# Optimization experiments

Measured on AMD Instinct MI355X. Metric: run time of the kernel, lower is better.

Reference implementation:

```python
import jax, jax.numpy as jnp
import numpy as np

B = 65536
IN = 512
SEQ = 4
LN_EPS = 1e-5


def _ln(x, g, b, eps=LN_EPS):
    # LayerNorm over last dim with affine params
    m = jnp.mean(x, axis=-1, keepdims=True)
    v = jnp.mean((x - m) ** 2, axis=-1, keepdims=True)
    return (x - m) * jax.lax.rsqrt(v + eps) * g + b


def setup_inputs() -> dict:
    key = jax.random.key(0)
    ks = jax.random.split(key, 24)

    def lin(k, shape, fan_in):
        return jax.random.normal(k, shape, jnp.float32) / np.sqrt(fan_in)

    return {
        "x": jax.random.normal(ks[0], (B, IN), jnp.float32),
        "history": jax.random.normal(ks[1], (B, SEQ * IN), jnp.float32),
        # gate network: (seq*in)->64->32
        "g1_w": lin(ks[2], (64, SEQ * IN), SEQ * IN), "g1_b": lin(ks[3], (64,), SEQ * IN),
        "g2_w": lin(ks[4], (32, 64), 64), "g2_b": lin(ks[5], (32,), 64),
        # base modulated layer in->128
        "base_w": lin(ks[6], (128, IN), IN), "base_b": lin(ks[7], (128,), IN),
        "ln1_g": jnp.ones((128,), jnp.float32), "ln1_b": jnp.zeros((128,), jnp.float32),
        # main network: NoisyLinear(eval) 128->64, LN(64), Linear 64->32
        "n1_w": lin(ks[8], (64, 128), 128), "n1_b": lin(ks[9], (64,), 128),
        "ln2_g": jnp.ones((64,), jnp.float32), "ln2_b": jnp.zeros((64,), jnp.float32),
        "m_w": lin(ks[10], (32, 64), 64), "m_b": lin(ks[11], (32,), 64),
        # value stream 32->16->1
        "v1_w": lin(ks[12], (16, 32), 32), "v1_b": lin(ks[13], (16,), 32),
        "v2_w": lin(ks[14], (1, 16), 16), "v2_b": lin(ks[15], (1,), 16),
        # advantage stream 32->16->4 (NoisyLinear in eval mode = mu only)
        "a1_w": lin(ks[16], (16, 32), 32), "a1_b": lin(ks[17], (16,), 32),
        "a2_w": lin(ks[18], (4, 16), 16), "a2_b": lin(ks[19], (4,), 16),
    }


def reference(x, history, g1_w, g1_b, g2_w, g2_b, base_w, base_b, ln1_g, ln1_b,
              n1_w, n1_b, ln2_g, ln2_b, m_w, m_b,
              v1_w, v1_b, v2_w, v2_b, a1_w, a1_b, a2_w, a2_b):
    # gate network
    h = jax.nn.relu(history @ g1_w.T + g1_b)
    gate_values = jax.nn.sigmoid(h @ g2_w.T + g2_b)            # [B, 32]
    mod = 0.7 + 0.3 * jnp.mean(gate_values, axis=1, keepdims=True)  # [B, 1]

    # per-sample scalar weight modulation: bmm(x, (mod*W)^T) == (x @ W^T) * mod
    x_gated = (x @ base_w.T) * mod + base_b                    # [B, 128]
    x_gated = _ln(jax.nn.relu(x_gated), ln1_g, ln1_b)

    # main network (NoisyLinear in eval mode -> mu weights)
    f = jax.nn.relu(x_gated @ n1_w.T + n1_b)
    f = _ln(f, ln2_g, ln2_b)
    features = jax.nn.relu(f @ m_w.T + m_b)                    # [B, 32]

    value = jax.nn.relu(features @ v1_w.T + v1_b) @ v2_w.T + v2_b    # [B, 1]
    advantage = jax.nn.relu(features @ a1_w.T + a1_b) @ a2_w.T + a2_b  # [B, 4]

    q_values = value + (advantage - jnp.mean(advantage, axis=1, keepdims=True))
    return q_values, gate_values
```

## Files before the change

kernel.cpp:

```cpp
#include <hip/hip_runtime.h>
#include <hip/hip_bf16.h>

typedef float f32x4 __attribute__((ext_vector_type(4)));
typedef __bf16 bf16x8 __attribute__((ext_vector_type(8)));
typedef unsigned int u32;
typedef u32 u32x4 __attribute__((ext_vector_type(4)));

#define PK1  0
#define PK2  131072
#define PK3  133120
#define PK4  264192
#define PK5  280576
#define PK6V 284672
#define PK6A 285696

__device__ __forceinline__ f32x4 mfma16(bf16x8 a, bf16x8 b, f32x4 c) {
    return __builtin_amdgcn_mfma_f32_16x16x32_bf16(a, b, c, 0, 0, 0);
}
__device__ __forceinline__ float redsum16(float v) {
    v += __shfl_xor(v, 1); v += __shfl_xor(v, 2);
    v += __shfl_xor(v, 4); v += __shfl_xor(v, 8);
    return v;
}
__device__ __forceinline__ unsigned short bfb(__bf16 b) {
    return __builtin_bit_cast(unsigned short, b);
}
__device__ __forceinline__ bf16x8 cvt8(f32x4 a, f32x4 b) {
    bf16x8 r;
    r[0]=(__bf16)a[0]; r[1]=(__bf16)a[1]; r[2]=(__bf16)a[2]; r[3]=(__bf16)a[3];
    r[4]=(__bf16)b[0]; r[5]=(__bf16)b[1]; r[6]=(__bf16)b[2]; r[7]=(__bf16)b[3];
    return r;
}
__device__ __forceinline__ void split8(f32x4 a, f32x4 b, bf16x8& h, bf16x8& l) {
    #pragma unroll
    for (int e=0;e<4;++e){ __bf16 hb=(__bf16)a[e]; h[e]=hb; l[e]=(__bf16)(a[e]-(float)hb); }
    #pragma unroll
    for (int e=0;e<4;++e){ __bf16 hb=(__bf16)b[e]; h[4+e]=hb; l[4+e]=(__bf16)(b[e]-(float)hb); }
}
__device__ __forceinline__ void unpack8(u32x4 w0, u32x4 w1, bf16x8& h, bf16x8& l) {
    u32 h0=(w0[0]&0xFFFFu)|(w0[1]<<16), h1=(w0[2]&0xFFFFu)|(w0[3]<<16);
    u32 h2=(w1[0]&0xFFFFu)|(w1[1]<<16), h3=(w1[2]&0xFFFFu)|(w1[3]<<16);
    u32 l0=(w0[0]>>16)|(w0[1]&0xFFFF0000u), l1=(w0[2]>>16)|(w0[3]&0xFFFF0000u);
    u32 l2=(w1[0]>>16)|(w1[1]&0xFFFF0000u), l3=(w1[2]>>16)|(w1[3]&0xFFFF0000u);
    u32x4 hv={h0,h1,h2,h3}, lv={l0,l1,l2,l3};
    h=__builtin_bit_cast(bf16x8,hv); l=__builtin_bit_cast(bf16x8,lv);
}

__device__ __forceinline__ void pack_plain(const float* __restrict__ W, __bf16* __restrict__ dst,
                                           int i, int K, int Nn) {
    int e=i&7, lane=(i>>3)&63, p=i>>9;
    int n=p%Nn, t=p/Nn;
    float v = W[(size_t)(n*16+(lane&15))*K + t*32 + (lane>>4)*8 + e];
    dst[i] = (__bf16)v;
}
__device__ __forceinline__ void pack_hilo(const float* __restrict__ W, __bf16* __restrict__ dst,
                                          int i, int K, int Nn) {
    int e=i&7, lane=(i>>3)&63, p=i>>9;
    int n=p%Nn, t=p/Nn;
    float v = W[(size_t)(n*16+(lane&15))*K + t*32 + (lane>>4)*8 + e];
    __bf16 h = (__bf16)v;
    dst[p*1024 + (i&511)]       = h;
    dst[p*1024 + 512 + (i&511)] = (__bf16)(v - (float)h);
}
__global__ void pack_weights(const float* g1w, const float* g2w, const float* bw,
                             const float* n1w, const float* mw, const float* v1w,
                             const float* a1w, __bf16* wsb) {
    int gi = blockIdx.x*256 + threadIdx.x;
    if      (gi < 131072) pack_plain(g1w, wsb+PK1, gi,          2048, 4);
    else if (gi < 133120) pack_plain(g2w, wsb+PK2, gi-131072,   64,   2);
    else if (gi < 198656) pack_hilo (bw,  wsb+PK3, gi-133120,   512,  8);
    else if (gi < 206848) pack_hilo (n1w, wsb+PK4, gi-198656,   128,  4);
    else if (gi < 208896) pack_hilo (mw,  wsb+PK5, gi-206848,   64,   2);
    else if (gi < 209408) pack_hilo (v1w, wsb+PK6V, gi-208896,  32,   1);
    else if (gi < 209920) pack_hilo (a1w, wsb+PK6A, gi-209408,  32,   1);
}

__global__ __launch_bounds__(256, 4)
void gated_dqn_main(const float* __restrict__ x,   const float* __restrict__ hist,
                    const float* __restrict__ g1b, const float* __restrict__ g2b,
                    const float* __restrict__ bb,  const float* __restrict__ ln1g,
                    const float* __restrict__ ln1b,const float* __restrict__ n1b,
                    const float* __restrict__ ln2g,const float* __restrict__ ln2b,
                    const float* __restrict__ mb,  const float* __restrict__ v1b,
                    const float* __restrict__ v2w, const float* __restrict__ v2b,
                    const float* __restrict__ a1b, const float* __restrict__ a2w,
                    const float* __restrict__ a2b, const __bf16* __restrict__ wsb,
                    float* __restrict__ qout, float* __restrict__ gateout)
{
    __shared__ __align__(16) float scr[4][2112];
    const int tid = threadIdx.x, lane = tid & 63, wv = tid >> 6;
    const int qq = lane >> 4, c = lane & 15;
    const int r0 = (blockIdx.x*4 + wv)*16;
    float*  myA = scr[wv];
    u32*    my  = (u32*)myA;
    __bf16* myb = (__bf16*)myA;
    const int swc = ((c >> 1) & 3) << 3;
    const int srl = lane >> 3, scl = lane & 7;

    f32x4 acc[4] = {};
    {
        const float* aRow0 = hist + (size_t)(r0 + srl)*2048 + scl*4;
        const float* aRow1 = hist + (size_t)(r0 + 8 + srl)*2048 + scl*4;
        f32x4 rg[8];
        #pragma unroll
        for (int q = 0; q < 4; ++q) {
            rg[q]   = *(const f32x4*)(aRow0 + q*32);
            rg[4+q] = *(const f32x4*)(aRow1 + q*32);
        }
        const __bf16* bB = wsb + PK1 + lane*8;
        bf16x8 cb0 = *(const bf16x8*)(bB),      cb1 = *(const bf16x8*)(bB+512);
        bf16x8 cb2 = *(const bf16x8*)(bB+1024), cb3 = *(const bf16x8*)(bB+1536);
        for (int g = 0; g < 16; ++g) {
            #pragma unroll
            for (int q = 0; q < 4; ++q) {
                *(f32x4*)&myA[srl*132     + q*32 + scl*4] = rg[q];
                *(f32x4*)&myA[(8+srl)*132 + q*32 + scl*4] = rg[4+q];
            }
            if (g + 1 < 16) {
                #pragma unroll
                for (int q = 0; q < 4; ++q) {
                    rg[q]   = *(const f32x4*)(aRow0 + (g+1)*128 + q*32);
                    rg[4+q] = *(const f32x4*)(aRow1 + (g+1)*128 + q*32);
                }
            }
            #pragma unroll
            for (int t = 0; t < 4; ++t) {
                int ktn = g*4 + t + 1; if (ktn > 63) ktn = 63;
                const __bf16* btn = bB + (size_t)ktn*2048;
                bf16x8 nb0 = *(const bf16x8*)(btn),      nb1 = *(const bf16x8*)(btn+512);
                bf16x8 nb2 = *(const bf16x8*)(btn+1024), nb3 = *(const bf16x8*)(btn+1536);
                f32x4 lo = *(const f32x4*)&myA[c*132 + t*32 + qq*8];
                f32x4 hi = *(const f32x4*)&myA[c*132 + t*32 + qq*8 + 4];
                bf16x8 af = cvt8(lo, hi);
                acc[0] = mfma16(af, cb0, acc[0]); acc[1] = mfma16(af, cb1, acc[1]);
                acc[2] = mfma16(af, cb2, acc[2]); acc[3] = mfma16(af, cb3, acc[3]);
                cb0 = nb0; cb1 = nb1; cb2 = nb2; cb3 = nb3;
            }
        }
        #pragma unroll
        for (int n = 0; n < 4; ++n) {
            float bv = g1b[n*16 + c];
            #pragma unroll
            for (int j = 0; j < 4; ++j) {
                int r = qq*4 + j, col = n*16 + c;
                myb[r*64 + (col ^ (((r>>1)&3)<<3))] = (__bf16)fmaxf(acc[n][j] + bv, 0.0f);
            }
        }
    }

    float mj[4];
    {
        const __bf16* bB = wsb + PK2 + lane*8;
        bf16x8 a0 = *(const bf16x8*)&myb[c*64 + ((qq*8) ^ swc)];
        bf16x8 a1 = *(const bf16x8*)&myb[c*64 + ((32 + qq*8) ^ swc)];
        bf16x8 b00 = *(const bf16x8*)(bB),      b01 = *(const bf16x8*)(bB+512);
        bf16x8 b10 = *(const bf16x8*)(bB+1024), b11 = *(const bf16x8*)(bB+1536);
        f32x4 ag0 = {}, ag1 = {};
        ag0 = mfma16(a0, b00, ag0); ag1 = mfma16(a0, b01, ag1);
        ag0 = mfma16(a1, b10, ag0); ag1 = mfma16(a1, b11, ag1);
        float s[4] = {0,0,0,0};
        #pragma unroll
        for (int n = 0; n < 2; ++n) {
            float bv = g2b[n*16 + c];
            f32x4 ag = n ? ag1 : ag0;
            #pragma unroll
            for (int j = 0; j < 4; ++j) {
                float gv = 1.0f / (1.0f + __expf(-(ag[j] + bv)));
                gateout[(size_t)(r0 + qq*4 + j)*32 + n*16 + c] = gv;
                s[j] += gv;
            }
        }
        #pragma unroll
        for (int j = 0; j < 4; ++j)
            mj[j] = 0.7f + 0.3f * redsum16(s[j]) * (1.0f/32.0f);
    }

    f32x4 a3[8] = {};
    {
        const float* aRow0 = x + (size_t)(r0 + srl)*512 + scl*4;
        const float* aRow1 = x + (size_t)(r0 + 8 + srl)*512 + scl*4;
        f32x4 rg[8];
        #pragma unroll
        for (int q = 0; q < 4; ++q) {
            rg[q]   = *(const f32x4*)(aRow0 + q*32);
            rg[4+q] = *(const f32x4*)(aRow1 + q*32);
        }
        for (int g = 0; g < 4; ++g) {
            #pragma unroll
            for (int q = 0; q < 4; ++q) {
                *(f32x4*)&myA[srl*132     + q*32 + scl*4] = rg[q];
                *(f32x4*)&myA[(8+srl)*132 + q*32 + scl*4] = rg[4+q];
            }
            if (g + 1 < 4) {
                #pragma unroll
                for (int q = 0; q < 4; ++q) {
                    rg[q]   = *(const f32x4*)(aRow0 + (g+1)*128 + q*32);
                    rg[4+q] = *(const f32x4*)(aRow1 + (g+1)*128 + q*32);
                }
            }
            #pragma unroll
            for (int t = 0; t < 4; ++t) {
                f32x4 lo = *(const f32x4*)&myA[c*132 + t*32 + qq*8];
                f32x4 hi = *(const f32x4*)&myA[c*132 + t*32 + qq*8 + 4];
                bf16x8 ah, al; split8(lo, hi, ah, al);
                int kt = g*4 + t;
                #pragma unroll
                for (int half = 0; half < 2; ++half) {
                    const __bf16* bt = wsb + PK3 + (size_t)(kt*16 + half*8)*512 + lane*8;
                    #pragma unroll
                    for (int n = 0; n < 4; ++n) {
                        bf16x8 bh = *(const bf16x8*)(bt + n*1024);
                        f32x4 a = a3[half*4 + n];
                        a = mfma16(ah, bh, a); a = mfma16(al, bh, a);
                        a3[half*4 + n] = a;
                    }
                }
            }
        }
        float s[4] = {0,0,0,0}, ss[4] = {0,0,0,0};
        #pragma unroll
        for (int n = 0; n < 8; ++n) {
            float bv = bb[n*16 + c];
            #pragma unroll
            for (int j = 0; j < 4; ++j) {
                float v = fmaxf(a3[n][j]*mj[j] + bv, 0.0f);
                a3[n][j] = v; s[j] += v; ss[j] += v*v;
            }
        }
        float mean[4], rstd[4];
        #pragma unroll
        for (int j = 0; j < 4; ++j) {
            float t = redsum16(s[j]), t2 = redsum16(ss[j]);
            float m = t * (1.0f/128.0f);
            mean[j] = m; rstd[j] = rsqrtf(t2*(1.0f/128.0f) - m*m + 1e-5f);
        }
        #pragma unroll
        for (int n = 0; n < 8; ++n) {
            float g = ln1g[n*16 + c], b2 = ln1b[n*16 + c];
            #pragma unroll
            for (int j = 0; j < 4; ++j) {
                int r = qq*4 + j, col = n*16 + c;
                float y = (a3[n][j] - mean[j]) * rstd[j] * g + b2;
                __bf16 hb = (__bf16)y; __bf16 lb = (__bf16)(y - (float)hb);
                my[r*128 + (col ^ (((r>>1)&3)<<3))] = (u32)bfb(hb) | ((u32)bfb(lb) << 16);
            }
        }
    }

    f32x4 a4[4] = {};
    {
        const __bf16* bB = wsb + PK4 + lane*8;
        #pragma unroll
        for (int t = 0; t < 4; ++t) {
            int base = c*128 + ((t*32 + qq*8) ^ swc);
            u32x4 w0 = *(const u32x4*)&my[base], w1 = *(const u32x4*)&my[base + 4];
            bf16x8 ah, al; unpack8(w0, w1, ah, al);
            const __bf16* bt = bB + t*4096;
            #pragma unroll
            for (int n = 0; n < 4; ++n) {
                bf16x8 bh = *(const bf16x8*)(bt + n*1024);
                f32x4 a = a4[n];
                a = mfma16(ah, bh, a); a = mfma16(al, bh, a);
                a4[n] = a;
            }
        }
        float s[4] = {0,0,0,0}, ss[4] = {0,0,0,0};
        #pragma unroll
        for (int n = 0; n < 4; ++n) {
            float bv = n1b[n*16 + c];
            #pragma unroll
            for (int j = 0; j < 4; ++j) {
                float v = fmaxf(a4[n][j] + bv, 0.0f);
                a4[n][j] = v; s[j] += v; ss[j] += v*v;
            }
        }
        float mean[4], rstd[4];
        #pragma unroll
        for (int j = 0; j < 4; ++j) {
            float t = redsum16(s[j]), t2 = redsum16(ss[j]);
            float m = t * (1.0f/64.0f);
            mean[j] = m; rstd[j] = rsqrtf(t2*(1.0f/64.0f) - m*m + 1e-5f);
        }
        #pragma unroll
        for (int n = 0; n < 4; ++n) {
            float g = ln2g[n*16 + c], b2 = ln2b[n*16 + c];
            #pragma unroll
            for (int j = 0; j < 4; ++j) {
                int r = qq*4 + j, col = n*16 + c;
                float y = (a4[n][j] - mean[j]) * rstd[j] * g + b2;
                __bf16 hb = (__bf16)y; __bf16 lb = (__bf16)(y - (float)hb);
                my[r*64 + (col ^ (((r>>1)&3)<<3))] = (u32)bfb(hb) | ((u32)bfb(lb) << 16);
            }
        }
    }

    {
        const __bf16* bB = wsb + PK5 + lane*8;
        f32x4 a5[2] = {};
        #pragma unroll
        for (int t = 0; t < 2; ++t) {
            int base = c*64 + ((t*32 + qq*8) ^ swc);
            u32x4 w0 = *(const u32x4*)&my[base], w1 = *(const u32x4*)&my[base + 4];
            bf16x8 ah, al; unpack8(w0, w1, ah, al);
            const __bf16* bt = bB + t*2048;
            #pragma unroll
            for (int n = 0; n < 2; ++n) {
                bf16x8 bh = *(const bf16x8*)(bt + n*1024);
                f32x4 a = a5[n];
                a = mfma16(ah, bh, a); a = mfma16(al, bh, a);
                a5[n] = a;
            }
        }
        #pragma unroll
        for (int n = 0; n < 2; ++n) {
            float bv = mb[n*16 + c];
            #pragma unroll
            for (int j = 0; j < 4; ++j) {
                int r = qq*4 + j, col = n*16 + c;
                float v = fmaxf(a5[n][j] + bv, 0.0f);
                __bf16 hb = (__bf16)v; __bf16 lb = (__bf16)(v - (float)hb);
                my[r*32 + (col ^ (((r>>1)&3)<<3))] = (u32)bfb(hb) | ((u32)bfb(lb) << 16);
            }
        }
    }

    {
        int base = c*32 + ((qq*8) ^ swc);
        u32x4 w0 = *(const u32x4*)&my[base], w1 = *(const u32x4*)&my[base + 4];
        bf16x8 ah, al; unpack8(w0, w1, ah, al);
        const __bf16* bv_ = wsb + PK6V + lane*8;
        const __bf16* ba_ = wsb + PK6A + lane*8;
        bf16x8 vh  = *(const bf16x8*)(bv_);
        bf16x8 ahw = *(const bf16x8*)(ba_);
        f32x4 av = {}, aa = {};
        av = mfma16(ah, vh, av);  av = mfma16(al, vh, av);
        aa = mfma16(ah, ahw, aa); aa = mfma16(al, ahw, aa);
        float v1bc = v1b[c], a1bc = a1b[c], w2 = v2w[c];
        float vb2 = v2b[0];
        float aw0 = a2w[c], aw1 = a2w[16+c], aw2 = a2w[32+c], aw3 = a2w[48+c];
        float ab0 = a2b[0], ab1 = a2b[1], ab2 = a2b[2], ab3 = a2b[3];
        #pragma unroll
        for (int j = 0; j < 4; ++j) {
            float hv = fmaxf(av[j] + v1bc, 0.0f);
            float ha = fmaxf(aa[j] + a1bc, 0.0f);
            float val = redsum16(hv * w2) + vb2;
            float d0 = redsum16(ha * aw0) + ab0;
            float d1 = redsum16(ha * aw1) + ab1;
            float d2 = redsum16(ha * aw2) + ab2;
            float d3 = redsum16(ha * aw3) + ab3;
            float ma = 0.25f * (d0 + d1 + d2 + d3);
            if (c == 0) {
                f32x4 qv = {val + d0 - ma, val + d1 - ma, val + d2 - ma, val + d3 - ma};
                *(f32x4*)(qout + (size_t)(r0 + qq*4 + j)*4) = qv;
            }
        }
    }
}

extern "C" void kernel_launch(void* const* d_in, const int* in_sizes, int n_in,
                              void* d_out, int out_size, void* d_ws, size_t ws_size,
                              hipStream_t stream) {
    (void)in_sizes; (void)n_in; (void)ws_size; (void)out_size;
    const float* x    = (const float*)d_in[0];
    const float* hist = (const float*)d_in[1];
    const float* g1w  = (const float*)d_in[2];
    const float* g1b  = (const float*)d_in[3];
    const float* g2w  = (const float*)d_in[4];
    const float* g2b  = (const float*)d_in[5];
    const float* bw   = (const float*)d_in[6];
    const float* bb   = (const float*)d_in[7];
    const float* ln1g = (const float*)d_in[8];
    const float* ln1b = (const float*)d_in[9];
    const float* n1w  = (const float*)d_in[10];
    const float* n1b  = (const float*)d_in[11];
    const float* ln2g = (const float*)d_in[12];
    const float* ln2b = (const float*)d_in[13];
    const float* mw   = (const float*)d_in[14];
    const float* mb   = (const float*)d_in[15];
    const float* v1w  = (const float*)d_in[16];
    const float* v1b  = (const float*)d_in[17];
    const float* v2w  = (const float*)d_in[18];
    const float* v2b  = (const float*)d_in[19];
    const float* a1w  = (const float*)d_in[20];
    const float* a1b  = (const float*)d_in[21];
    const float* a2w  = (const float*)d_in[22];
    const float* a2b  = (const float*)d_in[23];
    __bf16* wsb = (__bf16*)d_ws;
    float* qout = (float*)d_out;
    float* gateout = qout + (size_t)65536 * 4;

    pack_weights<<<dim3(820), dim3(256), 0, stream>>>(g1w, g2w, bw, n1w, mw, v1w, a1w, wsb);
    gated_dqn_main<<<dim3(1024), dim3(256), 0, stream>>>(
        x, hist, g1b, g2b, bb, ln1g, ln1b, n1b, ln2g, ln2b, mb,
        v1b, v2w, v2b, a1b, a2w, a2b, wsb, qout, gateout);
}
```

Measured before the change: 172.9 us.

## Process 32 rows per wave to reuse weight fragments across two row tiles

Each wave now computes two 16-row tiles, so every B-fragment (weight) load feeds two MFMA chains across all layers. The activation staging switches to 16 row-loads per lane and drops the XOR swizzle in favor of padded LDS rows. The grid is halved and launch bounds reduced to 2, with larger per-wave LDS and register footprints, trading occupancy for less weight traffic and more instruction-level parallelism.

```diff
diff --git a/kernel.cpp b/kernel.cpp
--- a/kernel.cpp
+++ b/kernel.cpp
@@ -75,7 +75,7 @@
     else if (gi < 209920) pack_hilo (a1w, wsb+PK6A, gi-209408,  32,   1);
 }
 
-__global__ __launch_bounds__(256, 4)
+__global__ __launch_bounds__(256, 2)
 void gated_dqn_main(const float* __restrict__ x,   const float* __restrict__ hist,
                     const float* __restrict__ g1b, const float* __restrict__ g2b,
                     const float* __restrict__ bb,  const float* __restrict__ ln1g,
@@ -87,41 +87,32 @@
                     const float* __restrict__ a2b, const __bf16* __restrict__ wsb,
                     float* __restrict__ qout, float* __restrict__ gateout)
 {
-    __shared__ __align__(16) float scr[4][2112];
+    __shared__ __align__(16) u32 scr[4][4224];
     const int tid = threadIdx.x, lane = tid & 63, wv = tid >> 6;
     const int qq = lane >> 4, c = lane & 15;
-    const int r0 = (blockIdx.x*4 + wv)*16;
-    float*  myA = scr[wv];
-    u32*    my  = (u32*)myA;
-    __bf16* myb = (__bf16*)myA;
-    const int swc = ((c >> 1) & 3) << 3;
-    const int srl = lane >> 3, scl = lane & 7;
-
-    f32x4 acc[4] = {};
-    {
-        const float* aRow0 = hist + (size_t)(r0 + srl)*2048 + scl*4;
-        const float* aRow1 = hist + (size_t)(r0 + 8 + srl)*2048 + scl*4;
-        f32x4 rg[8];
-        #pragma unroll
-        for (int q = 0; q < 4; ++q) {
-            rg[q]   = *(const f32x4*)(aRow0 + q*32);
-            rg[4+q] = *(const f32x4*)(aRow1 + q*32);
-        }
+    const int r0 = (blockIdx.x*4 + wv)*32;
+    u32*    my  = scr[wv];
+    float*  myA = (float*)my;
+    __bf16* myb = (__bf16*)my;
+    const int sr2 = lane >> 5, sc2 = lane & 31;
+
+    f32x4 acc1[2][4] = {};
+    {
+        const float* aBase = hist + (size_t)(r0 + sr2*16)*2048 + sc2*4;
+        f32x4 rg[16];
+        #pragma unroll
+        for (int i = 0; i < 16; ++i) rg[i] = *(const f32x4*)(aBase + (size_t)i*2048);
         const __bf16* bB = wsb + PK1 + lane*8;
         bf16x8 cb0 = *(const bf16x8*)(bB),      cb1 = *(const bf16x8*)(bB+512);
         bf16x8 cb2 = *(const bf16x8*)(bB+1024), cb3 = *(const bf16x8*)(bB+1536);
         for (int g = 0; g < 16; ++g) {
             #pragma unroll
-            for (int q = 0; q < 4; ++q) {
-                *(f32x4*)&myA[srl*132     + q*32 + scl*4] = rg[q];
-                *(f32x4*)&myA[(8+srl)*132 + q*32 + scl*4] = rg[4+q];
-            }
+            for (int i = 0; i < 16; ++i)
+                *(f32x4*)&myA[(i + sr2*16)*132 + sc2*4] = rg[i];
             if (g + 1 < 16) {
                 #pragma unroll
-                for (int q = 0; q < 4; ++q) {
-                    rg[q]   = *(const f32x4*)(aRow0 + (g+1)*128 + q*32);
-                    rg[4+q] = *(const f32x4*)(aRow1 + (g+1)*128 + q*32);
-                }
+                for (int i = 0; i < 16; ++i)
+                    rg[i] = *(const f32x4*)(aBase + (size_t)i*2048 + (g+1)*128);
             }
             #pragma unroll
             for (int t = 0; t < 4; ++t) {
@@ -129,229 +120,263 @@
                 const __bf16* btn = bB + (size_t)ktn*2048;
                 bf16x8 nb0 = *(const bf16x8*)(btn),      nb1 = *(const bf16x8*)(btn+512);
                 bf16x8 nb2 = *(const bf16x8*)(btn+1024), nb3 = *(const bf16x8*)(btn+1536);
-                f32x4 lo = *(const f32x4*)&myA[c*132 + t*32 + qq*8];
-                f32x4 hi = *(const f32x4*)&myA[c*132 + t*32 + qq*8 + 4];
-                bf16x8 af = cvt8(lo, hi);
-                acc[0] = mfma16(af, cb0, acc[0]); acc[1] = mfma16(af, cb1, acc[1]);
-                acc[2] = mfma16(af, cb2, acc[2]); acc[3] = mfma16(af, cb3, acc[3]);
+                #pragma unroll
+                for (int rt = 0; rt < 2; ++rt) {
+                    f32x4 lo = *(const f32x4*)&myA[(rt*16 + c)*132 + t*32 + qq*8];
+                    f32x4 hi = *(const f32x4*)&myA[(rt*16 + c)*132 + t*32 + qq*8 + 4];
+                    bf16x8 af = cvt8(lo, hi);
+                    acc1[rt][0] = mfma16(af, cb0, acc1[rt][0]);
+                    acc1[rt][1] = mfma16(af, cb1, acc1[rt][1]);
+                    acc1[rt][2] = mfma16(af, cb2, acc1[rt][2]);
+                    acc1[rt][3] = mfma16(af, cb3, acc1[rt][3]);
+                }
                 cb0 = nb0; cb1 = nb1; cb2 = nb2; cb3 = nb3;
             }
         }
         #pragma unroll
-        for (int n = 0; n < 4; ++n) {
-            float bv = g1b[n*16 + c];
-            #pragma unroll
-            for (int j = 0; j < 4; ++j) {
-                int r = qq*4 + j, col = n*16 + c;
-                myb[r*64 + (col ^ (((r>>1)&3)<<3))] = (__bf16)fmaxf(acc[n][j] + bv, 0.0f);
-            }
-        }
-    }
-
-    float mj[4];
+        for (int rt = 0; rt < 2; ++rt)
+            #pragma unroll
+            for (int n = 0; n < 4; ++n) {
+                float bv = g1b[n*16 + c];
+                #pragma unroll
+                for (int j = 0; j < 4; ++j) {
+                    int r = rt*16 + qq*4 + j;
+                    myb[r*136 + n*16 + c] = (__bf16)fmaxf(acc1[rt][n][j] + bv, 0.0f);
+                }
+            }
+    }
+
+    float mj[2][4];
     {
         const __bf16* bB = wsb + PK2 + lane*8;
-        bf16x8 a0 = *(const bf16x8*)&myb[c*64 + ((qq*8) ^ swc)];
-        bf16x8 a1 = *(const bf16x8*)&myb[c*64 + ((32 + qq*8) ^ swc)];
         bf16x8 b00 = *(const bf16x8*)(bB),      b01 = *(const bf16x8*)(bB+512);
         bf16x8 b10 = *(const bf16x8*)(bB+1024), b11 = *(const bf16x8*)(bB+1536);
-        f32x4 ag0 = {}, ag1 = {};
-        ag0 = mfma16(a0, b00, ag0); ag1 = mfma16(a0, b01, ag1);
-        ag0 = mfma16(a1, b10, ag0); ag1 = mfma16(a1, b11, ag1);
-        float s[4] = {0,0,0,0};
-        #pragma unroll
-        for (int n = 0; n < 2; ++n) {
-            float bv = g2b[n*16 + c];
-            f32x4 ag = n ? ag1 : ag0;
-            #pragma unroll
-            for (int j = 0; j < 4; ++j) {
-                float gv = 1.0f / (1.0f + __expf(-(ag[j] + bv)));
-                gateout[(size_t)(r0 + qq*4 + j)*32 + n*16 + c] = gv;
-                s[j] += gv;
-            }
-        }
-        #pragma unroll
-        for (int j = 0; j < 4; ++j)
-            mj[j] = 0.7f + 0.3f * redsum16(s[j]) * (1.0f/32.0f);
-    }
-
-    f32x4 a3[8] = {};
-    {
-        const float* aRow0 = x + (size_t)(r0 + srl)*512 + scl*4;
-        const float* aRow1 = x + (size_t)(r0 + 8 + srl)*512 + scl*4;
-        f32x4 rg[8];
-        #pragma unroll
-        for (int q = 0; q < 4; ++q) {
-            rg[q]   = *(const f32x4*)(aRow0 + q*32);
-            rg[4+q] = *(const f32x4*)(aRow1 + q*32);
-        }
+        #pragma unroll
+        for (int rt = 0; rt < 2; ++rt) {
+            bf16x8 a0 = *(const bf16x8*)&myb[(rt*16 + c)*136 + qq*8];
+            bf16x8 a1 = *(const bf16x8*)&myb[(rt*16 + c)*136 + 32 + qq*8];
+            f32x4 ag0 = {}, ag1 = {};
+            ag0 = mfma16(a0, b00, ag0); ag1 = mfma16(a0, b01, ag1);
+            ag0 = mfma16(a1, b10, ag0); ag1 = mfma16(a1, b11, ag1);
+            float s[4] = {0,0,0,0};
+            #pragma unroll
+            for (int n = 0; n < 2; ++n) {
+                float bv = g2b[n*16 + c];
+                f32x4 ag = n ? ag1 : ag0;
+                #pragma unroll
+                for (int j = 0; j < 4; ++j) {
+                    float gv = 1.0f / (1.0f + __expf(-(ag[j] + bv)));
+                    gateout[(size_t)(r0 + rt*16 + qq*4 + j)*32 + n*16 + c] = gv;
+                    s[j] += gv;
+                }
+            }
+            #pragma unroll
+            for (int j = 0; j < 4; ++j)
+                mj[rt][j] = 0.7f + 0.3f * redsum16(s[j]) * (1.0f/32.0f);
+        }
+    }
+
+    f32x4 a3[2][8] = {};
+    {
+        const float* aBase = x + (size_t)(r0 + sr2*16)*512 + sc2*4;
+        f32x4 rg[16];
+        #pragma unroll
+        for (int i = 0; i < 16; ++i) rg[i] = *(const f32x4*)(aBase + (size_t)i*512);
         for (int g = 0; g < 4; ++g) {
             #pragma unroll
-            for (int q = 0; q < 4; ++q) {
-                *(f32x4*)&myA[srl*132     + q*32 + scl*4] = rg[q];
-                *(f32x4*)&myA[(8+srl)*132 + q*32 + scl*4] = rg[4+q];
-            }
+            for (int i = 0; i < 16; ++i)
+                *(f32x4*)&myA[(i + sr2*16)*132 + sc2*4] = rg[i];
             if (g + 1 < 4) {
                 #pragma unroll
-                for (int q = 0; q < 4; ++q) {
-                    rg[q]   = *(const f32x4*)(aRow0 + (g+1)*128 + q*32);
-                    rg[4+q] = *(const f32x4*)(aRow1 + (g+1)*128 + q*32);
-                }
+                for (int i = 0; i < 16; ++i)
+                    rg[i] = *(const f32x4*)(aBase + (size_t)i*512 + (g+1)*128);
             }
             #pragma unroll
             for (int t = 0; t < 4; ++t) {
-                f32x4 lo = *(const f32x4*)&myA[c*132 + t*32 + qq*8];
-                f32x4 hi = *(const f32x4*)&myA[c*132 + t*32 + qq*8 + 4];
-                bf16x8 ah, al; split8(lo, hi, ah, al);
                 int kt = g*4 + t;
+                bf16x8 ah[2], al[2];
+                #pragma unroll
+                for (int rt = 0; rt < 2; ++rt) {
+                    f32x4 lo = *(const f32x4*)&myA[(rt*16 + c)*132 + t*32 + qq*8];
+                    f32x4 hi = *(const f32x4*)&myA[(rt*16 + c)*132 + t*32 + qq*8 + 4];
+                    split8(lo, hi, ah[rt], al[rt]);
+                }
                 #pragma unroll
                 for (int half = 0; half < 2; ++half) {
                     const __bf16* bt = wsb + PK3 + (size_t)(kt*16 + half*8)*512 + lane*8;
                     #pragma unroll
                     for (int n = 0; n < 4; ++n) {
                         bf16x8 bh = *(const bf16x8*)(bt + n*1024);
-                        f32x4 a = a3[half*4 + n];
-                        a = mfma16(ah, bh, a); a = mfma16(al, bh, a);
-                        a3[half*4 + n] = a;
+                        #pragma unroll
+                        for (int rt = 0; rt < 2; ++rt) {
+                            f32x4 a = a3[rt][half*4 + n];
+                            a = mfma16(ah[rt], bh, a); a = mfma16(al[rt], bh, a);
+                            a3[rt][half*4 + n] = a;
+                        }
                     }
                 }
             }
         }
-        float s[4] = {0,0,0,0}, ss[4] = {0,0,0,0};
-        #pragma unroll
-        for (int n = 0; n < 8; ++n) {
-            float bv = bb[n*16 + c];
+        #pragma unroll
+        for (int rt = 0; rt < 2; ++rt) {
+            float s[4] = {0,0,0,0}, ss[4] = {0,0,0,0};
+            #pragma unroll
+            for (int n = 0; n < 8; ++n) {
+                float bv = bb[n*16 + c];
+                #pragma unroll
+                for (int j = 0; j < 4; ++j) {
+                    float v = fmaxf(a3[rt][n][j]*mj[rt][j] + bv, 0.0f);
+                    a3[rt][n][j] = v; s[j] += v; ss[j] += v*v;
+                }
+            }
+            float mean[4], rstd[4];
             #pragma unroll
             for (int j = 0; j < 4; ++j) {
-                float v = fmaxf(a3[n][j]*mj[j] + bv, 0.0f);
-                a3[n][j] = v; s[j] += v; ss[j] += v*v;
-            }
-        }
-        float mean[4], rstd[4];
-        #pragma unroll
-        for (int j = 0; j < 4; ++j) {
-            float t = redsum16(s[j]), t2 = redsum16(ss[j]);
-            float m = t * (1.0f/128.0f);
-            mean[j] = m; rstd[j] = rsqrtf(t2*(1.0f/128.0f) - m*m + 1e-5f);
-        }
-        #pragma unroll
-        for (int n = 0; n < 8; ++n) {
-            float g = ln1g[n*16 + c], b2 = ln1b[n*16 + c];
-            #pragma unroll
-            for (int j = 0; j < 4; ++j) {
-                int r = qq*4 + j, col = n*16 + c;
-                float y = (a3[n][j] - mean[j]) * rstd[j] * g + b2;
-                __bf16 hb = (__bf16)y; __bf16 lb = (__bf16)(y - (float)hb);
-                my[r*128 + (col ^ (((r>>1)&3)<<3))] = (u32)bfb(hb) | ((u32)bfb(lb) << 16);
-            }
-        }
-    }
-
-    f32x4 a4[4] = {};
+                float t = redsum16(s[j]), t2 = redsum16(ss[j]);
+                float m = t * (1.0f/128.0f);
+                mean[j] = m; rstd[j] = rsqrtf(t2*(1.0f/128.0f) - m*m + 1e-5f);
+            }
+            #pragma unroll
+            for (int n = 0; n < 8; ++n) {
+                float g = ln1g[n*16 + c], b2 = ln1b[n*16 + c];
+                #pragma unroll
+                for (int j = 0; j < 4; ++j) {
+                    int r = rt*16 + qq*4 + j;
+                    float y = (a3[rt][n][j] - mean[j]) * rstd[j] * g + b2;
+                    __bf16 hb = (__bf16)y; __bf16 lb = (__bf16)(y - (float)hb);
+                    my[r*132 + n*16 + c] = (u32)bfb(hb) | ((u32)bfb(lb) << 16);
+                }
+            }
+        }
+    }
+
+    f32x4 a4[2][4] = {};
     {
         const __bf16* bB = wsb + PK4 + lane*8;
         #pragma unroll
         for (int t = 0; t < 4; ++t) {
-            int base = c*128 + ((t*32 + qq*8) ^ swc);
-            u32x4 w0 = *(const u32x4*)&my[base], w1 = *(const u32x4*)&my[base + 4];
-            bf16x8 ah, al; unpack8(w0, w1, ah, al);
+            bf16x8 ah[2], al[2];
+            #pragma unroll
+            for (int rt = 0; rt < 2; ++rt) {
+                int base = (rt*16 + c)*132 + t*32 + qq*8;
+                u32x4 w0 = *(const u32x4*)&my[base], w1 = *(const u32x4*)&my[base + 4];
+                unpack8(w0, w1, ah[rt], al[rt]);
+            }
             const __bf16* bt = bB + t*4096;
             #pragma unroll
             for (int n = 0; n < 4; ++n) {
                 bf16x8 bh = *(const bf16x8*)(bt + n*1024);
-                f32x4 a = a4[n];
-                a = mfma16(ah, bh, a); a = mfma16(al, bh, a);
-                a4[n] = a;
-            }
-        }
-        float s[4] = {0,0,0,0}, ss[4] = {0,0,0,0};
-        #pragma unroll
-        for (int n = 0; n < 4; ++n) {
-            float bv = n1b[n*16 + c];
+                #pragma unroll
+                for (int rt = 0; rt < 2; ++rt) {
+                    f32x4 a = a4[rt][n];
+                    a = mfma16(ah[rt], bh, a); a = mfma16(al[rt], bh, a);
+                    a4[rt][n] = a;
+                }
+            }
+        }
+        #pragma unroll
+        for (int rt = 0; rt < 2; ++rt) {
+            float s[4] = {0,0,0,0}, ss[4] = {0,0,0,0};
+            #pragma unroll
+            for (int n = 0; n < 4; ++n) {
+                float bv = n1b[n*16 + c];
+                #pragma unroll
+                for (int j = 0; j < 4; ++j) {
+                    float v = fmaxf(a4[rt][n][j] + bv, 0.0f);
+                    a4[rt][n][j] = v; s[j] += v; ss[j] += v*v;
+                }
+            }
+            float mean[4], rstd[4];
             #pragma unroll
             for (int j = 0; j < 4; ++j) {
-                float v = fmaxf(a4[n][j] + bv, 0.0f);
-                a4[n][j] = v; s[j] += v; ss[j] += v*v;
-            }
-        }
-        float mean[4], rstd[4];
-        #pragma unroll
-        for (int j = 0; j < 4; ++j) {
-            float t = redsum16(s[j]), t2 = redsum16(ss[j]);
-            float m = t * (1.0f/64.0f);
-            mean[j] = m; rstd[j] = rsqrtf(t2*(1.0f/64.0f) - m*m + 1e-5f);
-        }
-        #pragma unroll
-        for (int n = 0; n < 4; ++n) {
-            float g = ln2g[n*16 + c], b2 = ln2b[n*16 + c];
-            #pragma unroll
-            for (int j = 0; j < 4; ++j) {
-                int r = qq*4 + j, col = n*16 + c;
-                float y = (a4[n][j] - mean[j]) * rstd[j] * g + b2;
-                __bf16 hb = (__bf16)y; __bf16 lb = (__bf16)(y - (float)hb);
-                my[r*64 + (col ^ (((r>>1)&3)<<3))] = (u32)bfb(hb) | ((u32)bfb(lb) << 16);
+                float t = redsum16(s[j]), t2 = redsum16(ss[j]);
+                float m = t * (1.0f/64.0f);
+                mean[j] = m; rstd[j] = rsqrtf(t2*(1.0f/64.0f) - m*m + 1e-5f);
+            }
+            #pragma unroll
+            for (int n = 0; n < 4; ++n) {
+                float g = ln2g[n*16 + c], b2 = ln2b[n*16 + c];
+                #pragma unroll
+                for (int j = 0; j < 4; ++j) {
+                    int r = rt*16 + qq*4 + j;
+                    float y = (a4[rt][n][j] - mean[j]) * rstd[j] * g + b2;
+                    __bf16 hb = (__bf16)y; __bf16 lb = (__bf16)(y - (float)hb);
+                    my[r*132 + n*16 + c] = (u32)bfb(hb) | ((u32)bfb(lb) << 16);
+                }
             }
         }
     }
 
     {
         const __bf16* bB = wsb + PK5 + lane*8;
-        f32x4 a5[2] = {};
+        f32x4 a5[2][2] = {};
         #pragma unroll
         for (int t = 0; t < 2; ++t) {
-            int base = c*64 + ((t*32 + qq*8) ^ swc);
-            u32x4 w0 = *(const u32x4*)&my[base], w1 = *(const u32x4*)&my[base + 4];
-            bf16x8 ah, al; unpack8(w0, w1, ah, al);
+            bf16x8 ah[2], al[2];
+            #pragma unroll
+            for (int rt = 0; rt < 2; ++rt) {
+                int base = (rt*16 + c)*132 + t*32 + qq*8;
+                u32x4 w0 = *(const u32x4*)&my[base], w1 = *(const u32x4*)&my[base + 4];
+                unpack8(w0, w1, ah[rt], al[rt]);
+            }
             const __bf16* bt = bB + t*2048;
             #pragma unroll
             for (int n = 0; n < 2; ++n) {
                 bf16x8 bh = *(const bf16x8*)(bt + n*1024);
-                f32x4 a = a5[n];
-                a = mfma16(ah, bh, a); a = mfma16(al, bh, a);
-                a5[n] = a;
-            }
-        }
-        #pragma unroll
-        for (int n = 0; n < 2; ++n) {
-            float bv = mb[n*16 + c];
-            #pragma unroll
-            for (int j = 0; j < 4; ++j) {
-                int r = qq*4 + j, col = n*16 + c;
-                float v = fmaxf(a5[n][j] + bv, 0.0f);
-                __bf16 hb = (__bf16)v; __bf16 lb = (__bf16)(v - (float)hb);
-                my[r*32 + (col ^ (((r>>1)&3)<<3))] = (u32)bfb(hb) | ((u32)bfb(lb) << 16);
-            }
-        }
-    }
-
-    {
-        int base = c*32 + ((qq*8) ^ swc);
-        u32x4 w0 = *(const u32x4*)&my[base], w1 = *(const u32x4*)&my[base + 4];
-        bf16x8 ah, al; unpack8(w0, w1, ah, al);
+                #pragma unroll
+                for (int rt = 0; rt < 2; ++rt) {
+                    f32x4 a = a5[rt][n];
+                    a = mfma16(ah[rt], bh, a); a = mfma16(al[rt], bh, a);
+                    a5[rt][n] = a;
+                }
+            }
+        }
+        #pragma unroll
+        for (int rt = 0; rt < 2; ++rt)
+            #pragma unroll
+            for (int n = 0; n < 2; ++n) {
+                float bv = mb[n*16 + c];
+                #pragma unroll
+                for (int j = 0; j < 4; ++j) {
+                    int r = rt*16 + qq*4 + j;
+                    float v = fmaxf(a5[rt][n][j] + bv, 0.0f);
+                    __bf16 hb = (__bf16)v; __bf16 lb = (__bf16)(v - (float)hb);
+                    my[r*132 + n*16 + c] = (u32)bfb(hb) | ((u32)bfb(lb) << 16);
+                }
+            }
+    }
+
+    {
         const __bf16* bv_ = wsb + PK6V + lane*8;
         const __bf16* ba_ = wsb + PK6A + lane*8;
         bf16x8 vh  = *(const bf16x8*)(bv_);
         bf16x8 ahw = *(const bf16x8*)(ba_);
-        f32x4 av = {}, aa = {};
-        av = mfma16(ah, vh, av);  av = mfma16(al, vh, av);
-        aa = mfma16(ah, ahw, aa); aa = mfma16(al, ahw, aa);
         float v1bc = v1b[c], a1bc = a1b[c], w2 = v2w[c];
         float vb2 = v2b[0];
         float aw0 = a2w[c], aw1 = a2w[16+c], aw2 = a2w[32+c], aw3 = a2w[48+c];
         float ab0 = a2b[0], ab1 = a2b[1], ab2 = a2b[2], ab3 = a2b[3];
         #pragma unroll
-        for (int j = 0; j < 4; ++j) {
-            float hv = fmaxf(av[j] + v1bc, 0.0f);
-            float ha = fmaxf(aa[j] + a1bc, 0.0f);
-            float val = redsum16(hv * w2) + vb2;
-            float d0 = redsum16(ha * aw0) + ab0;
-            float d1 = redsum16(ha * aw1) + ab1;
-            float d2 = redsum16(ha * aw2) + ab2;
-            float d3 = redsum16(ha * aw3) + ab3;
-            float ma = 0.25f * (d0 + d1 + d2 + d3);
-            if (c == 0) {
-                f32x4 qv = {val + d0 - ma, val + d1 - ma, val + d2 - ma, val + d3 - ma};
-                *(f32x4*)(qout + (size_t)(r0 + qq*4 + j)*4) = qv;
+        for (int rt = 0; rt < 2; ++rt) {
+            int base = (rt*16 + c)*132 + qq*8;
+            u32x4 w0 = *(const u32x4*)&my[base], w1 = *(const u32x4*)&my[base + 4];
+            bf16x8 ah, al; unpack8(w0, w1, ah, al);
+            f32x4 av = {}, aa = {};
+            av = mfma16(ah, vh, av);  av = mfma16(al, vh, av);
+            aa = mfma16(ah, ahw, aa); aa = mfma16(al, ahw, aa);
+            #pragma unroll
+            for (int j = 0; j < 4; ++j) {
+                float hv = fmaxf(av[j] + v1bc, 0.0f);
+                float ha = fmaxf(aa[j] + a1bc, 0.0f);
+                float val = redsum16(hv * w2) + vb2;
+                float d0 = redsum16(ha * aw0) + ab0;
+                float d1 = redsum16(ha * aw1) + ab1;
+                float d2 = redsum16(ha * aw2) + ab2;
+                float d3 = redsum16(ha * aw3) + ab3;
+                float ma = 0.25f * (d0 + d1 + d2 + d3);
+                if (c == 0) {
+                    f32x4 qv = {val + d0 - ma, val + d1 - ma, val + d2 - ma, val + d3 - ma};
+                    *(f32x4*)(qout + (size_t)(r0 + rt*16 + qq*4 + j)*4) = qv;
+                }
             }
         }
     }
@@ -390,7 +415,7 @@
     float* gateout = qout + (size_t)65536 * 4;
 
     pack_weights<<<dim3(820), dim3(256), 0, stream>>>(g1w, g2w, bw, n1w, mw, v1w, a1w, wsb);
-    gated_dqn_main<<<dim3(1024), dim3(256), 0, stream>>>(
+    gated_dqn_main<<<dim3(512), dim3(256), 0, stream>>>(
         x, hist, g1b, g2b, bb, ln1g, ln1b, n1b, ln2g, ln2b, mb,
         v1b, v2w, v2b, a1b, a2w, a2b, wsb, qout, gateout);
 }
```

After: 175.5 us. About the same (+1.5%).

## Stream history and x tiles into LDS with async global_load_lds double-buffering

Applied to the files above, without the earlier changes.

Replaces the register-staged global→LDS copies of the history and x row tiles with direct global_load_lds transfers into a double-buffered, XOR-swizzled LDS layout. Explicit vmcnt waits overlap the next chunk's load with the current chunk's MFMAs, and the loops are fully unrolled with B fragments loaded per step. The aim is to cut VGPR pressure and the store/load round trip through registers, making the kernel more memory-streaming friendly. It depends on hand-placed waitcnt counts staying correct alongside the compiler's own B-fragment loads. It also drops the previous one-step-ahead B prefetch.

```diff
diff --git a/kernel.cpp b/kernel.cpp
--- a/kernel.cpp
+++ b/kernel.cpp
@@ -44,6 +44,11 @@
     u32 l2=(w1[0]>>16)|(w1[1]&0xFFFF0000u), l3=(w1[2]>>16)|(w1[3]&0xFFFF0000u);
     u32x4 hv={h0,h1,h2,h3}, lv={l0,l1,l2,l3};
     h=__builtin_bit_cast(bf16x8,hv); l=__builtin_bit_cast(bf16x8,lv);
+}
+__device__ __forceinline__ void gl16(const void* g, void* l) {
+    __builtin_amdgcn_global_load_lds(
+        (const __attribute__((address_space(1))) void*)g,
+        (__attribute__((address_space(3))) void*)l, 16, 0, 0);
 }
 
 __device__ __forceinline__ void pack_plain(const float* __restrict__ W, __bf16* __restrict__ dst,
@@ -90,69 +95,72 @@
     __shared__ __align__(16) float scr[4][2112];
     const int tid = threadIdx.x, lane = tid & 63, wv = tid >> 6;
     const int qq = lane >> 4, c = lane & 15;
+    const int c7 = c & 7;
     const int r0 = (blockIdx.x*4 + wv)*16;
     float*  myA = scr[wv];
     u32*    my  = (u32*)myA;
-    __bf16* myb = (__bf16*)myA;
+    char*   ldsA = (char*)myA;
     const int swc = ((c >> 1) & 3) << 3;
-    const int srl = lane >> 3, scl = lane & 7;
 
     f32x4 acc[4] = {};
     {
-        const float* aRow0 = hist + (size_t)(r0 + srl)*2048 + scl*4;
-        const float* aRow1 = hist + (size_t)(r0 + 8 + srl)*2048 + scl*4;
-        f32x4 rg[8];
-        #pragma unroll
-        for (int q = 0; q < 4; ++q) {
-            rg[q]   = *(const f32x4*)(aRow0 + q*32);
-            rg[4+q] = *(const f32x4*)(aRow1 + q*32);
-        }
+        const int glr = lane >> 4, gls = lane & 15;
+        const float* gA[4];
+        #pragma unroll
+        for (int i = 0; i < 4; ++i) {
+            int lr = i*4 + glr;
+            gA[i] = hist + (size_t)(r0 + lr)*2048 + (gls ^ (lr & 7))*4;
+        }
+        #pragma unroll
+        for (int i = 0; i < 4; ++i) gl16(gA[i], ldsA + i*1024);
         const __bf16* bB = wsb + PK1 + lane*8;
-        bf16x8 cb0 = *(const bf16x8*)(bB),      cb1 = *(const bf16x8*)(bB+512);
-        bf16x8 cb2 = *(const bf16x8*)(bB+1024), cb3 = *(const bf16x8*)(bB+1536);
-        for (int g = 0; g < 16; ++g) {
-            #pragma unroll
-            for (int q = 0; q < 4; ++q) {
-                *(f32x4*)&myA[srl*132     + q*32 + scl*4] = rg[q];
-                *(f32x4*)&myA[(8+srl)*132 + q*32 + scl*4] = rg[4+q];
-            }
-            if (g + 1 < 16) {
+        #pragma unroll
+        for (int t = 0; t < 32; ++t) {
+            bf16x8 Bf[2][4];
+            #pragma unroll
+            for (int ktl = 0; ktl < 2; ++ktl)
                 #pragma unroll
-                for (int q = 0; q < 4; ++q) {
-                    rg[q]   = *(const f32x4*)(aRow0 + (g+1)*128 + q*32);
-                    rg[4+q] = *(const f32x4*)(aRow1 + (g+1)*128 + q*32);
-                }
-            }
-            #pragma unroll
-            for (int t = 0; t < 4; ++t) {
-                int ktn = g*4 + t + 1; if (ktn > 63) ktn = 63;
-                const __bf16* btn = bB + (size_t)ktn*2048;
-                bf16x8 nb0 = *(const bf16x8*)(btn),      nb1 = *(const bf16x8*)(btn+512);
-                bf16x8 nb2 = *(const bf16x8*)(btn+1024), nb3 = *(const bf16x8*)(btn+1536);
-                f32x4 lo = *(const f32x4*)&myA[c*132 + t*32 + qq*8];
-                f32x4 hi = *(const f32x4*)&myA[c*132 + t*32 + qq*8 + 4];
+                for (int n = 0; n < 4; ++n)
+                    Bf[ktl][n] = *(const bf16x8*)(bB + (size_t)(t*2 + ktl)*2048 + n*512);
+            if (t + 1 < 32) {
+                char* dst = ldsA + ((t+1)&1)*4096;
+                #pragma unroll
+                for (int i = 0; i < 4; ++i) gl16(gA[i] + (t+1)*64, dst + i*1024);
+                asm volatile("s_waitcnt vmcnt(4)" ::: "memory");
+            } else {
+                asm volatile("s_waitcnt vmcnt(0)" ::: "memory");
+            }
+            const float* buf = myA + (t&1)*1024;
+            #pragma unroll
+            for (int ktl = 0; ktl < 2; ++ktl) {
+                int k0 = ktl*8 + qq*2;
+                f32x4 lo = *(const f32x4*)&buf[c*64 + ((k0    ) ^ c7)*4];
+                f32x4 hi = *(const f32x4*)&buf[c*64 + ((k0 + 1) ^ c7)*4];
                 bf16x8 af = cvt8(lo, hi);
-                acc[0] = mfma16(af, cb0, acc[0]); acc[1] = mfma16(af, cb1, acc[1]);
-                acc[2] = mfma16(af, cb2, acc[2]); acc[3] = mfma16(af, cb3, acc[3]);
-                cb0 = nb0; cb1 = nb1; cb2 = nb2; cb3 = nb3;
-            }
-        }
+                acc[0] = mfma16(af, Bf[ktl][0], acc[0]);
+                acc[1] = mfma16(af, Bf[ktl][1], acc[1]);
+                acc[2] = mfma16(af, Bf[ktl][2], acc[2]);
+                acc[3] = mfma16(af, Bf[ktl][3], acc[3]);
+            }
+        }
+        __bf16* hB = (__bf16*)(myA + 1024);
         #pragma unroll
         for (int n = 0; n < 4; ++n) {
             float bv = g1b[n*16 + c];
             #pragma unroll
             for (int j = 0; j < 4; ++j) {
                 int r = qq*4 + j, col = n*16 + c;
-                myb[r*64 + (col ^ (((r>>1)&3)<<3))] = (__bf16)fmaxf(acc[n][j] + bv, 0.0f);
+                hB[r*64 + (col ^ (((r>>1)&3)<<3))] = (__bf16)fmaxf(acc[n][j] + bv, 0.0f);
             }
         }
     }
 
     float mj[4];
     {
+        const __bf16* hB = (const __bf16*)(myA + 1024);
         const __bf16* bB = wsb + PK2 + lane*8;
-        bf16x8 a0 = *(const bf16x8*)&myb[c*64 + ((qq*8) ^ swc)];
-        bf16x8 a1 = *(const bf16x8*)&myb[c*64 + ((32 + qq*8) ^ swc)];
+        bf16x8 a0 = *(const bf16x8*)&hB[c*64 + ((qq*8) ^ swc)];
+        bf16x8 a1 = *(const bf16x8*)&hB[c*64 + ((32 + qq*8) ^ swc)];
         bf16x8 b00 = *(const bf16x8*)(bB),      b01 = *(const bf16x8*)(bB+512);
         bf16x8 b10 = *(const bf16x8*)(bB+1024), b11 = *(const bf16x8*)(bB+1536);
         f32x4 ag0 = {}, ag1 = {};
@@ -177,44 +185,37 @@
 
     f32x4 a3[8] = {};
     {
-        const float* aRow0 = x + (size_t)(r0 + srl)*512 + scl*4;
-        const float* aRow1 = x + (size_t)(r0 + 8 + srl)*512 + scl*4;
-        f32x4 rg[8];
-        #pragma unroll
-        for (int q = 0; q < 4; ++q) {
-            rg[q]   = *(const f32x4*)(aRow0 + q*32);
-            rg[4+q] = *(const f32x4*)(aRow1 + q*32);
-        }
-        for (int g = 0; g < 4; ++g) {
-            #pragma unroll
-            for (int q = 0; q < 4; ++q) {
-                *(f32x4*)&myA[srl*132     + q*32 + scl*4] = rg[q];
-                *(f32x4*)&myA[(8+srl)*132 + q*32 + scl*4] = rg[4+q];
-            }
-            if (g + 1 < 4) {
+        const int glr3 = lane >> 3, gls3 = lane & 7;
+        const float* gX[2];
+        #pragma unroll
+        for (int i = 0; i < 2; ++i) {
+            int lr = i*8 + glr3;
+            gX[i] = x + (size_t)(r0 + lr)*512 + (gls3 ^ (lr & 7))*4;
+        }
+        #pragma unroll
+        for (int i = 0; i < 2; ++i) gl16(gX[i], ldsA + i*1024);
+        #pragma unroll
+        for (int t = 0; t < 16; ++t) {
+            bf16x8 Bh[8];
+            #pragma unroll
+            for (int n = 0; n < 8; ++n)
+                Bh[n] = *(const bf16x8*)(wsb + PK3 + (size_t)(t*16 + n*2)*512 + lane*8);
+            if (t + 1 < 16) {
+                char* dst = ldsA + ((t+1)&1)*2048;
                 #pragma unroll
-                for (int q = 0; q < 4; ++q) {
-                    rg[q]   = *(const f32x4*)(aRow0 + (g+1)*128 + q*32);
-                    rg[4+q] = *(const f32x4*)(aRow1 + (g+1)*128 + q*32);
-                }
-            }
-            #pragma unroll
-            for (int t = 0; t < 4; ++t) {
-                f32x4 lo = *(const f32x4*)&myA[c*132 + t*32 + qq*8];
-                f32x4 hi = *(const f32x4*)&myA[c*132 + t*32 + qq*8 + 4];
-                bf16x8 ah, al; split8(lo, hi, ah, al);
-                int kt = g*4 + t;
-                #pragma unroll
-                for (int half = 0; half < 2; ++half) {
-                    const __bf16* bt = wsb + PK3 + (size_t)(kt*16 + half*8)*512 + lane*8;
-                    #pragma unroll
-                    for (int n = 0; n < 4; ++n) {
-                        bf16x8 bh = *(const bf16x8*)(bt + n*1024);
-                        f32x4 a = a3[half*4 + n];
-                        a = mfma16(ah, bh, a); a = mfma16(al, bh, a);
-                        a3[half*4 + n] = a;
-                    }
-                }
+                for (int i = 0; i < 2; ++i) gl16(gX[i] + (t+1)*32, dst + i*1024);
+                asm volatile("s_waitcnt vmcnt(2)" ::: "memory");
+            } else {
+                asm volatile("s_waitcnt vmcnt(0)" ::: "memory");
+            }
+            const float* buf = myA + (t&1)*512;
+            f32x4 lo = *(const f32x4*)&buf[c*32 + ((qq*2    ) ^ c7)*4];
+            f32x4 hi = *(const f32x4*)&buf[c*32 + ((qq*2 + 1) ^ c7)*4];
+            bf16x8 ah, al; split8(lo, hi, ah, al);
+            #pragma unroll
+            for (int n = 0; n < 8; ++n) {
+                a3[n] = mfma16(ah, Bh[n], a3[n]);
+                a3[n] = mfma16(al, Bh[n], a3[n]);
             }
         }
         float s[4] = {0,0,0,0}, ss[4] = {0,0,0,0};
```

Result: slower. 186.7 us (+8.0%).

## Widen staged chunks, row-per-load global reads, and loop two tiles per block

Applied to the files above, without the earlier changes.

The input staging for history and x now loads 256-float chunks, with one full row segment per instruction across the wavefront (16 rows of 1 KB contiguous each), instead of 128-float chunks split across 8 lanes per row. The LDS stride becomes 260 floats, so the per-wave scratch roughly doubles. Each block now processes two 16-row tiles per wave in a loop, with the grid halved to 512 and launch bounds relaxed to 2 blocks per SM. The aim is more bytes in flight per load and fewer staging iterations for the bandwidth-bound history read. In exchange, the larger LDS footprint and register buffer (16 f32x4) reduce occupancy.

```diff
diff --git a/kernel.cpp b/kernel.cpp
--- a/kernel.cpp
+++ b/kernel.cpp
@@ -13,6 +13,8 @@
 #define PK5  280576
 #define PK6V 284672
 #define PK6A 285696
+
+#define ASTR 260
 
 __device__ __forceinline__ f32x4 mfma16(bf16x8 a, bf16x8 b, f32x4 c) {
     return __builtin_amdgcn_mfma_f32_16x16x32_bf16(a, b, c, 0, 0, 0);
@@ -75,7 +77,7 @@
     else if (gi < 209920) pack_hilo (a1w, wsb+PK6A, gi-209408,  32,   1);
 }
 
-__global__ __launch_bounds__(256, 4)
+__global__ __launch_bounds__(256, 2)
 void gated_dqn_main(const float* __restrict__ x,   const float* __restrict__ hist,
                     const float* __restrict__ g1b, const float* __restrict__ g2b,
                     const float* __restrict__ bb,  const float* __restrict__ ln1g,
@@ -87,50 +89,43 @@
                     const float* __restrict__ a2b, const __bf16* __restrict__ wsb,
                     float* __restrict__ qout, float* __restrict__ gateout)
 {
-    __shared__ __align__(16) float scr[4][2112];
+    __shared__ __align__(16) float scr[4][16*ASTR];
     const int tid = threadIdx.x, lane = tid & 63, wv = tid >> 6;
     const int qq = lane >> 4, c = lane & 15;
-    const int r0 = (blockIdx.x*4 + wv)*16;
     float*  myA = scr[wv];
     u32*    my  = (u32*)myA;
     __bf16* myb = (__bf16*)myA;
     const int swc = ((c >> 1) & 3) << 3;
-    const int srl = lane >> 3, scl = lane & 7;
+
+    for (int it = 0; it < 2; ++it) {
+    const int r0 = ((it*512 + blockIdx.x)*4 + wv)*16;
 
     f32x4 acc[4] = {};
     {
-        const float* aRow0 = hist + (size_t)(r0 + srl)*2048 + scl*4;
-        const float* aRow1 = hist + (size_t)(r0 + 8 + srl)*2048 + scl*4;
-        f32x4 rg[8];
-        #pragma unroll
-        for (int q = 0; q < 4; ++q) {
-            rg[q]   = *(const f32x4*)(aRow0 + q*32);
-            rg[4+q] = *(const f32x4*)(aRow1 + q*32);
-        }
+        const float* aG = hist + (size_t)r0*2048 + lane*4;
+        f32x4 rg[16];
+        #pragma unroll
+        for (int i = 0; i < 16; ++i) rg[i] = *(const f32x4*)(aG + (size_t)i*2048);
         const __bf16* bB = wsb + PK1 + lane*8;
         bf16x8 cb0 = *(const bf16x8*)(bB),      cb1 = *(const bf16x8*)(bB+512);
         bf16x8 cb2 = *(const bf16x8*)(bB+1024), cb3 = *(const bf16x8*)(bB+1536);
-        for (int g = 0; g < 16; ++g) {
-            #pragma unroll
-            for (int q = 0; q < 4; ++q) {
-                *(f32x4*)&myA[srl*132     + q*32 + scl*4] = rg[q];
-                *(f32x4*)&myA[(8+srl)*132 + q*32 + scl*4] = rg[4+q];
-            }
-            if (g + 1 < 16) {
+        for (int g = 0; g < 8; ++g) {
+            #pragma unroll
+            for (int i = 0; i < 16; ++i)
+                *(f32x4*)&myA[i*ASTR + lane*4] = rg[i];
+            if (g + 1 < 8) {
                 #pragma unroll
-                for (int q = 0; q < 4; ++q) {
-                    rg[q]   = *(const f32x4*)(aRow0 + (g+1)*128 + q*32);
-                    rg[4+q] = *(const f32x4*)(aRow1 + (g+1)*128 + q*32);
-                }
-            }
-            #pragma unroll
-            for (int t = 0; t < 4; ++t) {
-                int ktn = g*4 + t + 1; if (ktn > 63) ktn = 63;
+                for (int i = 0; i < 16; ++i)
+                    rg[i] = *(const f32x4*)(aG + (size_t)i*2048 + (g+1)*256);
+            }
+            #pragma unroll
+            for (int t = 0; t < 8; ++t) {
+                int ktn = g*8 + t + 1; if (ktn > 63) ktn = 63;
                 const __bf16* btn = bB + (size_t)ktn*2048;
                 bf16x8 nb0 = *(const bf16x8*)(btn),      nb1 = *(const bf16x8*)(btn+512);
                 bf16x8 nb2 = *(const bf16x8*)(btn+1024), nb3 = *(const bf16x8*)(btn+1536);
-                f32x4 lo = *(const f32x4*)&myA[c*132 + t*32 + qq*8];
-                f32x4 hi = *(const f32x4*)&myA[c*132 + t*32 + qq*8 + 4];
+                f32x4 lo = *(const f32x4*)&myA[c*ASTR + t*32 + qq*8];
+                f32x4 hi = *(const f32x4*)&myA[c*ASTR + t*32 + qq*8 + 4];
                 bf16x8 af = cvt8(lo, hi);
                 acc[0] = mfma16(af, cb0, acc[0]); acc[1] = mfma16(af, cb1, acc[1]);
                 acc[2] = mfma16(af, cb2, acc[2]); acc[3] = mfma16(af, cb3, acc[3]);
@@ -177,33 +172,26 @@
 
     f32x4 a3[8] = {};
     {
-        const float* aRow0 = x + (size_t)(r0 + srl)*512 + scl*4;
-        const float* aRow1 = x + (size_t)(r0 + 8 + srl)*512 + scl*4;
-        f32x4 rg[8];
-        #pragma unroll
-        for (int q = 0; q < 4; ++q) {
-            rg[q]   = *(const f32x4*)(aRow0 + q*32);
-            rg[4+q] = *(const f32x4*)(aRow1 + q*32);
-        }
-        for (int g = 0; g < 4; ++g) {
-            #pragma unroll
-            for (int q = 0; q < 4; ++q) {
-                *(f32x4*)&myA[srl*132     + q*32 + scl*4] = rg[q];
-                *(f32x4*)&myA[(8+srl)*132 + q*32 + scl*4] = rg[4+q];
-            }
-            if (g + 1 < 4) {
+        const float* aG = x + (size_t)r0*512 + lane*4;
+        f32x4 rg[16];
+        #pragma unroll
+        for (int i = 0; i < 16; ++i) rg[i] = *(const f32x4*)(aG + (size_t)i*512);
+        #pragma unroll
+        for (int g = 0; g < 2; ++g) {
+            #pragma unroll
+            for (int i = 0; i < 16; ++i)
+                *(f32x4*)&myA[i*ASTR + lane*4] = rg[i];
+            if (g + 1 < 2) {
                 #pragma unroll
-                for (int q = 0; q < 4; ++q) {
-                    rg[q]   = *(const f32x4*)(aRow0 + (g+1)*128 + q*32);
-                    rg[4+q] = *(const f32x4*)(aRow1 + (g+1)*128 + q*32);
-                }
-            }
-            #pragma unroll
-            for (int t = 0; t < 4; ++t) {
-                f32x4 lo = *(const f32x4*)&myA[c*132 + t*32 + qq*8];
-                f32x4 hi = *(const f32x4*)&myA[c*132 + t*32 + qq*8 + 4];
+                for (int i = 0; i < 16; ++i)
+                    rg[i] = *(const f32x4*)(aG + (size_t)i*512 + 256);
+            }
+            #pragma unroll
+            for (int t = 0; t < 8; ++t) {
+                f32x4 lo = *(const f32x4*)&myA[c*ASTR + t*32 + qq*8];
+                f32x4 hi = *(const f32x4*)&myA[c*ASTR + t*32 + qq*8 + 4];
                 bf16x8 ah, al; split8(lo, hi, ah, al);
-                int kt = g*4 + t;
+                int kt = g*8 + t;
                 #pragma unroll
                 for (int half = 0; half < 2; ++half) {
                     const __bf16* bt = wsb + PK3 + (size_t)(kt*16 + half*8)*512 + lane*8;
@@ -354,6 +342,7 @@
                 *(f32x4*)(qout + (size_t)(r0 + qq*4 + j)*4) = qv;
             }
         }
+    }
     }
 }
 
@@ -390,7 +379,7 @@
     float* gateout = qout + (size_t)65536 * 4;
 
     pack_weights<<<dim3(820), dim3(256), 0, stream>>>(g1w, g2w, bw, n1w, mw, v1w, a1w, wsb);
-    gated_dqn_main<<<dim3(1024), dim3(256), 0, stream>>>(
+    gated_dqn_main<<<dim3(512), dim3(256), 0, stream>>>(
         x, hist, g1b, g2b, bb, ln1g, ln1b, n1b, ln2g, ln2b, mb,
         v1b, v2w, v2b, a1b, a2w, a2b, wsb, qout, gateout);
 }
```

New measurement: 439.3 us. 2.54x slower.
